# Performance work log

Measured on AMD Instinct MI355X. Metric: run time of the kernel, lower is better.

## Reference

```python
import jax, jax.numpy as jnp
import numpy as np

B, H, W, D = 64, 32, 32, 64
K = 1024  # codebook_size


def setup_inputs() -> dict:
    key = jax.random.key(0)
    kz, ke = jax.random.split(key)
    z = jax.random.normal(kz, (B, H, W, D), dtype=jnp.float32)
    embeddings = 0.02 * jax.random.normal(ke, (K, D), dtype=jnp.float32)
    return {"z": z, "embeddings": embeddings}


def reference(z, embeddings):
    # Flatten spatial/batch dims: (N, D) with N = B*H*W
    z_flat = z.reshape(-1, z.shape[-1])
    # Squared euclidean distances via ||a||^2 + ||b||^2 - 2 a.b  -> (N, K)
    distances = (jnp.sum(z_flat ** 2, axis=1, keepdims=True)
                 + jnp.sum(embeddings ** 2, axis=1)
                 - 2.0 * jnp.dot(z_flat, embeddings.T))
    indices = jnp.argmin(distances, axis=1)  # (N,)
    quantized = embeddings[indices].reshape(z.shape)  # (B, H, W, D)
    indices = indices.reshape(z.shape[0], z.shape[1], z.shape[2])  # (B, H, W)
    return quantized, indices
```

## Files before the change

kernel.cpp:

```cpp
#include <hip/hip_runtime.h>

#define NPTS   65536
#define DDIM   64
#define KCODES 1024
#define QOUT_ELEMS (NPTS * DDIM)

typedef _Float16 half8    __attribute__((ext_vector_type(8)));
typedef float    floatx16 __attribute__((ext_vector_type(16)));
typedef unsigned int uint;

#define AS1 __attribute__((address_space(1)))
#define AS3 __attribute__((address_space(3)))

#define WS_EHP   0
#define WS_ELP   (128*1024)
#define WS_E2    (256*1024)

static __device__ __forceinline__ void gl_lds16(const void* g, void* l) {
    __builtin_amdgcn_global_load_lds((const AS1 uint*)g, (AS3 uint*)l, 16, 0, 0);
}

__global__ void eprep_kernel(const float* __restrict__ emb, char* __restrict__ ws) {
    const int tid = threadIdx.x;
    const int w = tid >> 6, d = tid & 63;
    const int k = blockIdx.x * 4 + w;
    float v = emb[(size_t)k * DDIM + d];
    _Float16 h = (_Float16)v;
    _Float16 l = (_Float16)(v - (float)h);
    size_t off = (size_t)(k >> 5) * 4096 + (size_t)(d >> 3) * 512
               + (size_t)(k & 31) * 16 + (size_t)(d & 7) * 2;
    *(_Float16*)(ws + WS_EHP + off) = h;
    *(_Float16*)(ws + WS_ELP + off) = l;
    float s = v * v;
    #pragma unroll
    for (int m = 1; m < 64; m <<= 1) s += __shfl_xor(s, m, 64);
    if (d == 0) ((float*)(ws + WS_E2))[k] = s;
}

#define MFMA(A,B,C) __builtin_amdgcn_mfma_f32_32x32x16_f16(A,B,C,0,0,0)

__global__ __launch_bounds__(256, 2) void vq_kernel(
    const float* __restrict__ z,
    const char* __restrict__ ws_c,
    const float* __restrict__ emb,
    float* __restrict__ out)
{
    const int tid  = threadIdx.x;
    const int lane = tid & 63;
    const int w    = __builtin_amdgcn_readfirstlane(tid >> 6);
    const int col  = lane & 31;
    const int sel8 = lane >> 5;
    const int pgrp = blockIdx.x;

    __shared__ char  ebuf[2][8192];
    __shared__ float lds_e2[1024];
    __shared__ int   s_final[128];

    const int pt = pgrp * 128 + w * 32 + col;
    half8 ah[4], al[4];
    {
        const float* zrow = z + (size_t)pt * DDIM + sel8 * 8;
        #pragma unroll
        for (int ks = 0; ks < 4; ++ks) {
            float4 u0 = *(const float4*)(zrow + ks * 16);
            float4 u1 = *(const float4*)(zrow + ks * 16 + 4);
            float tv[8] = {u0.x, u0.y, u0.z, u0.w, u1.x, u1.y, u1.z, u1.w};
            #pragma unroll
            for (int j = 0; j < 8; ++j) {
                float a = -2.0f * tv[j];
                _Float16 hh = (_Float16)a;
                ah[ks][j] = hh;
                al[ks][j] = (_Float16)(a - (float)hh);
            }
        }
    }

    const floatx16 zeroC = {};

    float best[16];
    int   bt[16];
    #pragma unroll
    for (int r = 0; r < 16; ++r) { best[r] = 3.4e38f; bt[r] = 0; }

    gl_lds16(ws_c + WS_E2 + w * 1024 + lane * 16, (char*)lds_e2 + w * 1024);

    const int opnd = w >> 1, hsel = w & 1;
    const char* gsrc = ws_c + (opnd ? WS_ELP : WS_EHP) + hsel * 2048 + lane * 16;
    char* ld0 = &ebuf[0][0] + opnd * 4096 + hsel * 2048 + lane * 16;
    char* ld1 = &ebuf[1][0] + opnd * 4096 + hsel * 2048 + lane * 16;

#define STAGE(BUF, T) do {                                                    \
    const char* _s = gsrc + (size_t)(T) * 4096;                               \
    char* _d = (BUF) ? ld1 : ld0;                                             \
    gl_lds16(_s,        _d);                                                  \
    gl_lds16(_s + 1024, _d + 1024);                                           \
} while (0)

    const int myoff = sel8 * 512 + col * 16;
    const char* fb0 = &ebuf[0][0] + myoff;
    const char* fb1 = &ebuf[1][0] + myoff;

#define READF(BUF, T, BH, BL, E2) do {                                        \
    const char* _b = (BUF) ? fb1 : fb0;                                       \
    _Pragma("unroll")                                                         \
    for (int ks = 0; ks < 4; ++ks) {                                          \
        BH[ks] = *(const half8*)(_b + ks * 1024);                             \
        BL[ks] = *(const half8*)(_b + 4096 + ks * 1024);                      \
    }                                                                         \
    E2 = lds_e2[(T) * 32 + col];                                              \
} while (0)

#define COMP(T, BH, BL, E2) do {                                              \
    __builtin_amdgcn_s_setprio(1);                                            \
    floatx16 c0 = MFMA(ah[0], BH[0], zeroC);                                  \
    floatx16 c1 = MFMA(ah[0], BL[0], zeroC);                                  \
    c0 = MFMA(ah[1], BH[1], c0);  c1 = MFMA(ah[1], BL[1], c1);                \
    c0 = MFMA(ah[2], BH[2], c0);  c1 = MFMA(ah[2], BL[2], c1);                \
    c0 = MFMA(ah[3], BH[3], c0);  c1 = MFMA(ah[3], BL[3], c1);                \
    c0 = MFMA(al[0], BH[0], c0);  c1 = MFMA(al[2], BH[2], c1);                \
    c0 = MFMA(al[1], BH[1], c0);  c1 = MFMA(al[3], BH[3], c1);                \
    __builtin_amdgcn_s_setprio(0);                                            \
    _Pragma("unroll")                                                         \
    for (int r = 0; r < 16; ++r) {                                            \
        float d = (c0[r] + c1[r]) + (E2);                                     \
        bool c = d < best[r];               \
        best[r] = c ? d   : best[r];                                          \
        bt[r]   = c ? (T) : bt[r];                                            \
    }                                                                         \
} while (0)

    half8 bhA[4], blA[4], bhB[4], blB[4];
    float e2A, e2B;

    STAGE(0, 0);
    __syncthreads();
    READF(0, 0, bhA, blA, e2A);
    STAGE(1, 1);

    for (int t = 0; t < 32; t += 2) {
        __syncthreads();
        READF(1, t + 1, bhB, blB, e2B);
        if (t + 2 < 32) STAGE(0, t + 2);
        COMP(t, bhA, blA, e2A);

        __syncthreads();
        if (t + 2 < 32) READF(0, t + 2, bhA, blA, e2A);
        if (t + 3 < 32) STAGE(1, t + 3);
        COMP(t + 1, bhB, blB, e2B);
    }
#undef STAGE
#undef READF
#undef COMP

    int code[16];
    #pragma unroll
    for (int r = 0; r < 16; ++r) code[r] = bt[r] * 32 + col;
    #pragma unroll
    for (int m = 1; m < 32; m <<= 1) {
        #pragma unroll
        for (int r = 0; r < 16; ++r) {
            float ov = __shfl_xor(best[r], m, 64);
            int   oc = __shfl_xor(code[r], m, 64);
            bool c = (ov < best[r]) || (ov == best[r] && oc < code[r]);
            best[r] = c ? ov : best[r];
            code[r] = c ? oc : code[r];
        }
    }
    if (col == 0) {
        #pragma unroll
        for (int r = 0; r < 16; ++r) {
            int row = (r & 3) + 8 * (r >> 2) + 4 * sel8;
            s_final[w * 32 + row] = code[r];
        }
    }
    __syncthreads();

    if (tid < 128)
        out[QOUT_ELEMS + (size_t)pgrp * 128 + tid] = (float)s_final[tid];
    float4* outq = (float4*)out;
    const float4* emb4 = (const float4*)emb;
    #pragma unroll
    for (int it = 0; it < 8; ++it) {
        int f  = it * 256 + tid;
        int p  = f >> 4;
        int d4 = f & 15;
        int ks = s_final[p];
        outq[((size_t)pgrp * 128 + p) * (DDIM / 4) + d4] =
            emb4[(size_t)ks * (DDIM / 4) + d4];
    }
}

extern "C" void kernel_launch(void* const* d_in, const int* in_sizes, int n_in,
                              void* d_out, int out_size, void* d_ws, size_t ws_size,
                              hipStream_t stream) {
    const float* z   = (const float*)d_in[0];
    const float* emb = (const float*)d_in[1];
    float* out = (float*)d_out;
    char* ws = (char*)d_ws;

    eprep_kernel<<<KCODES / 4, 256, 0, stream>>>(emb, ws);
    vq_kernel<<<NPTS / 128, 256, 0, stream>>>(z, ws, emb, out);
}
```

Before: 103.2 us.

## Deepen codebook LDS prefetch to a four-buffer pipeline with explicit vmcnt waits

```diff
diff --git a/kernel.cpp b/kernel.cpp
--- a/kernel.cpp
+++ b/kernel.cpp
@@ -52,7 +52,7 @@
     const int sel8 = lane >> 5;
     const int pgrp = blockIdx.x;
 
-    __shared__ char  ebuf[2][8192];
+    __shared__ char  ebuf[4][8192];
     __shared__ float lds_e2[1024];
     __shared__ int   s_final[128];
 
@@ -74,6 +74,8 @@
             }
         }
     }
+    asm volatile("s_waitcnt vmcnt(0)" ::: "memory");
+    __builtin_amdgcn_sched_barrier(0);
 
     const floatx16 zeroC = {};
 
@@ -82,26 +84,21 @@
     #pragma unroll
     for (int r = 0; r < 16; ++r) { best[r] = 3.4e38f; bt[r] = 0; }
 
-    gl_lds16(ws_c + WS_E2 + w * 1024 + lane * 16, (char*)lds_e2 + w * 1024);
-
     const int opnd = w >> 1, hsel = w & 1;
     const char* gsrc = ws_c + (opnd ? WS_ELP : WS_EHP) + hsel * 2048 + lane * 16;
-    char* ld0 = &ebuf[0][0] + opnd * 4096 + hsel * 2048 + lane * 16;
-    char* ld1 = &ebuf[1][0] + opnd * 4096 + hsel * 2048 + lane * 16;
+    char* lbase = &ebuf[0][0] + opnd * 4096 + hsel * 2048;
 
 #define STAGE(BUF, T) do {                                                    \
     const char* _s = gsrc + (size_t)(T) * 4096;                               \
-    char* _d = (BUF) ? ld1 : ld0;                                             \
+    char* _d = lbase + (BUF) * 8192;                                          \
     gl_lds16(_s,        _d);                                                  \
     gl_lds16(_s + 1024, _d + 1024);                                           \
 } while (0)
 
     const int myoff = sel8 * 512 + col * 16;
-    const char* fb0 = &ebuf[0][0] + myoff;
-    const char* fb1 = &ebuf[1][0] + myoff;
 
 #define READF(BUF, T, BH, BL, E2) do {                                        \
-    const char* _b = (BUF) ? fb1 : fb0;                                       \
+    const char* _b = &ebuf[BUF][0] + myoff;                                   \
     _Pragma("unroll")                                                         \
     for (int ks = 0; ks < 4; ++ks) {                                          \
         BH[ks] = *(const half8*)(_b + ks * 1024);                             \
@@ -129,28 +126,54 @@
     }                                                                         \
 } while (0)
 
+#define WAITBAR(N) do {                                                       \
+    asm volatile("s_waitcnt vmcnt(" #N ") lgkmcnt(0)" ::: "memory");          \
+    __builtin_amdgcn_sched_barrier(0);                                        \
+    __builtin_amdgcn_s_barrier();                                             \
+    __builtin_amdgcn_sched_barrier(0);                                        \
+} while (0)
+
     half8 bhA[4], blA[4], bhB[4], blB[4];
     float e2A, e2B;
 
+    gl_lds16(ws_c + WS_E2 + w * 1024 + lane * 16, (char*)lds_e2 + w * 1024);
     STAGE(0, 0);
-    __syncthreads();
+    STAGE(1, 1);
+    STAGE(2, 2);
+    WAITBAR(4);
     READF(0, 0, bhA, blA, e2A);
-    STAGE(1, 1);
-
-    for (int t = 0; t < 32; t += 2) {
-        __syncthreads();
-        READF(1, t + 1, bhB, blB, e2B);
-        if (t + 2 < 32) STAGE(0, t + 2);
+    STAGE(3, 3);
+
+    #pragma unroll 1
+    for (int t = 0; t < 28; t += 2) {
+        WAITBAR(4);
+        READF((t + 1) & 3, t + 1, bhB, blB, e2B);
+        STAGE((t + 4) & 3, t + 4);
         COMP(t, bhA, blA, e2A);
 
-        __syncthreads();
-        if (t + 2 < 32) READF(0, t + 2, bhA, blA, e2A);
-        if (t + 3 < 32) STAGE(1, t + 3);
+        WAITBAR(4);
+        READF((t + 2) & 3, t + 2, bhA, blA, e2A);
+        STAGE((t + 5) & 3, t + 5);
         COMP(t + 1, bhB, blB, e2B);
     }
+
+    WAITBAR(4);
+    READF(29 & 3, 29, bhB, blB, e2B);
+    COMP(28, bhA, blA, e2A);
+
+    WAITBAR(2);
+    READF(30 & 3, 30, bhA, blA, e2A);
+    COMP(29, bhB, blB, e2B);
+
+    WAITBAR(0);
+    READF(31 & 3, 31, bhB, blB, e2B);
+    COMP(30, bhA, blA, e2A);
+
+    COMP(31, bhB, blB, e2B);
 #undef STAGE
 #undef READF
 #undef COMP
+#undef WAITBAR
 
     int code[16];
     #pragma unroll
```

Result: faster. 99.78 us (-3.3%).

## Split codebook across wave pairs per block, halving points per block

Applied to the files above, without the earlier changes.

```diff
diff --git a/kernel.cpp b/kernel.cpp
--- a/kernel.cpp
+++ b/kernel.cpp
@@ -39,24 +39,29 @@
 
 #define MFMA(A,B,C) __builtin_amdgcn_mfma_f32_32x32x16_f16(A,B,C,0,0,0)
 
-__global__ __launch_bounds__(256, 2) void vq_kernel(
+__global__ __launch_bounds__(256, 4) void vq_kernel(
     const float* __restrict__ z,
     const char* __restrict__ ws_c,
     const float* __restrict__ emb,
     float* __restrict__ out)
 {
-    const int tid  = threadIdx.x;
-    const int lane = tid & 63;
-    const int w    = __builtin_amdgcn_readfirstlane(tid >> 6);
-    const int col  = lane & 31;
-    const int sel8 = lane >> 5;
-    const int pgrp = blockIdx.x;
-
-    __shared__ char  ebuf[2][8192];
+    const int tid   = threadIdx.x;
+    const int lane  = tid & 63;
+    const int w     = __builtin_amdgcn_readfirstlane(tid >> 6);
+    const int col   = lane & 31;
+    const int sel8  = lane >> 5;
+    const int pgrp  = blockIdx.x;
+    const int pair  = w >> 1;
+    const int phalf = w & 1;
+    const int tbase = pair * 16;
+
+    __shared__ char  ebuf[2][2][8192];
     __shared__ float lds_e2[1024];
-    __shared__ int   s_final[128];
-
-    const int pt = pgrp * 128 + w * 32 + col;
+    __shared__ float sbest[2][64];
+    __shared__ int   scode[2][64];
+    __shared__ int   s_final[64];
+
+    const int pt = pgrp * 64 + phalf * 32 + col;
     half8 ah[4], al[4];
     {
         const float* zrow = z + (size_t)pt * DDIM + sel8 * 8;
@@ -74,40 +79,37 @@
             }
         }
     }
+    asm volatile("s_waitcnt vmcnt(0)" ::: "memory");
+    __builtin_amdgcn_sched_barrier(0);
 
     const floatx16 zeroC = {};
-
     float best[16];
     int   bt[16];
     #pragma unroll
     for (int r = 0; r < 16; ++r) { best[r] = 3.4e38f; bt[r] = 0; }
 
-    gl_lds16(ws_c + WS_E2 + w * 1024 + lane * 16, (char*)lds_e2 + w * 1024);
-
-    const int opnd = w >> 1, hsel = w & 1;
-    const char* gsrc = ws_c + (opnd ? WS_ELP : WS_EHP) + hsel * 2048 + lane * 16;
-    char* ld0 = &ebuf[0][0] + opnd * 4096 + hsel * 2048 + lane * 16;
-    char* ld1 = &ebuf[1][0] + opnd * 4096 + hsel * 2048 + lane * 16;
-
-#define STAGE(BUF, T) do {                                                    \
-    const char* _s = gsrc + (size_t)(T) * 4096;                               \
-    char* _d = (BUF) ? ld1 : ld0;                                             \
+    const char* gsrc = ws_c + (phalf ? WS_ELP : WS_EHP) + lane * 16;
+    char* lbase = &ebuf[pair][0][0] + phalf * 4096 + lane * 16;
+
+#define STAGE(SLOT, T) do {                                                   \
+    const char* _s = gsrc + (size_t)(tbase + (T)) * 4096;                     \
+    char* _d = lbase + (SLOT) * 8192;                                         \
     gl_lds16(_s,        _d);                                                  \
     gl_lds16(_s + 1024, _d + 1024);                                           \
+    gl_lds16(_s + 2048, _d + 2048);                                           \
+    gl_lds16(_s + 3072, _d + 3072);                                           \
 } while (0)
 
     const int myoff = sel8 * 512 + col * 16;
-    const char* fb0 = &ebuf[0][0] + myoff;
-    const char* fb1 = &ebuf[1][0] + myoff;
-
-#define READF(BUF, T, BH, BL, E2) do {                                        \
-    const char* _b = (BUF) ? fb1 : fb0;                                       \
+
+#define READF(SLOT, T, BH, BL, E2) do {                                       \
+    const char* _b = &ebuf[pair][SLOT][0] + myoff;                            \
     _Pragma("unroll")                                                         \
     for (int ks = 0; ks < 4; ++ks) {                                          \
         BH[ks] = *(const half8*)(_b + ks * 1024);                             \
         BL[ks] = *(const half8*)(_b + 4096 + ks * 1024);                      \
     }                                                                         \
-    E2 = lds_e2[(T) * 32 + col];                                              \
+    E2 = lds_e2[(tbase + (T)) * 32 + col];                                    \
 } while (0)
 
 #define COMP(T, BH, BL, E2) do {                                              \
@@ -124,33 +126,43 @@
     for (int r = 0; r < 16; ++r) {                                            \
         float d = (c0[r] + c1[r]) + (E2);                                     \
         bool c = d < best[r];               \
-        best[r] = c ? d   : best[r];                                          \
-        bt[r]   = c ? (T) : bt[r];                                            \
+        best[r] = c ? d          : best[r];                                   \
+        bt[r]   = c ? (tbase+(T)) : bt[r];                                    \
     }                                                                         \
+} while (0)
+
+#define WAITBAR do {                                                          \
+    asm volatile("s_waitcnt vmcnt(0) lgkmcnt(0)" ::: "memory");               \
+    __builtin_amdgcn_sched_barrier(0);                                        \
+    __builtin_amdgcn_s_barrier();                                             \
+    __builtin_amdgcn_sched_barrier(0);                                        \
 } while (0)
 
     half8 bhA[4], blA[4], bhB[4], blB[4];
     float e2A, e2B;
 
+    gl_lds16(ws_c + WS_E2 + w * 1024 + lane * 16, (char*)lds_e2 + w * 1024);
     STAGE(0, 0);
-    __syncthreads();
+    WAITBAR;
     READF(0, 0, bhA, blA, e2A);
     STAGE(1, 1);
 
-    for (int t = 0; t < 32; t += 2) {
-        __syncthreads();
-        READF(1, t + 1, bhB, blB, e2B);
-        if (t + 2 < 32) STAGE(0, t + 2);
+    #pragma unroll 1
+    for (int t = 0; t < 16; t += 2) {
+        WAITBAR;
+        READF((t + 1) & 1, t + 1, bhB, blB, e2B);
+        if (t + 2 < 16) STAGE((t + 2) & 1, t + 2);
         COMP(t, bhA, blA, e2A);
 
-        __syncthreads();
-        if (t + 2 < 32) READF(0, t + 2, bhA, blA, e2A);
-        if (t + 3 < 32) STAGE(1, t + 3);
+        WAITBAR;
+        if (t + 2 < 16) READF((t + 2) & 1, t + 2, bhA, blA, e2A);
+        if (t + 3 < 16) STAGE((t + 3) & 1, t + 3);
         COMP(t + 1, bhB, blB, e2B);
     }
 #undef STAGE
 #undef READF
 #undef COMP
+#undef WAITBAR
 
     int code[16];
     #pragma unroll
@@ -170,22 +182,29 @@
         #pragma unroll
         for (int r = 0; r < 16; ++r) {
             int row = (r & 3) + 8 * (r >> 2) + 4 * sel8;
-            s_final[w * 32 + row] = code[r];
+            sbest[pair][phalf * 32 + row] = best[r];
+            scode[pair][phalf * 32 + row] = code[r];
         }
     }
     __syncthreads();
 
-    if (tid < 128)
-        out[QOUT_ELEMS + (size_t)pgrp * 128 + tid] = (float)s_final[tid];
+    if (tid < 64) {
+        float d0 = sbest[0][tid], d1 = sbest[1][tid];
+        s_final[tid] = (d1 < d0) ? scode[1][tid] : scode[0][tid];
+    }
+    __syncthreads();
+
+    if (tid < 64)
+        out[QOUT_ELEMS + (size_t)pgrp * 64 + tid] = (float)s_final[tid];
     float4* outq = (float4*)out;
     const float4* emb4 = (const float4*)emb;
     #pragma unroll
-    for (int it = 0; it < 8; ++it) {
+    for (int it = 0; it < 4; ++it) {
         int f  = it * 256 + tid;
         int p  = f >> 4;
         int d4 = f & 15;
         int ks = s_final[p];
-        outq[((size_t)pgrp * 128 + p) * (DDIM / 4) + d4] =
+        outq[((size_t)pgrp * 64 + p) * (DDIM / 4) + d4] =
             emb4[(size_t)ks * (DDIM / 4) + d4];
     }
 }
@@ -199,5 +218,5 @@
     char* ws = (char*)d_ws;
 
     eprep_kernel<<<KCODES / 4, 256, 0, stream>>>(emb, ws);
-    vq_kernel<<<NPTS / 128, 256, 0, stream>>>(z, ws, emb, out);
-}
+    vq_kernel<<<NPTS / 64, 256, 0, stream>>>(z, ws, emb, out);
+}
```

New measurement: 244.4 us. +137.0%, slower.
